# Kernel optimization log

Hardware: AMD Instinct MI355X
Metric: run time of the kernel (lower is better)

## Reference

```python
import jax, jax.numpy as jnp
import numpy as np

# Model dims (see init_kwargs)
B, S, H = 1, 1024, 2048
NH, NKV, HD = 16, 4, 128       # query heads, kv heads (GQA), head dim
RD = 64                        # partial rotary dim
E, TOPK, I = 8, 2, 1024        # experts, top-k, expert intermediate
EPS = 1e-6
THETA = 1000000.0


def setup_inputs() -> dict:
    key = jax.random.key(0)
    ks = jax.random.split(key, 12)
    s = 0.02  # init scale
    return {
        "hidden_states": jax.random.normal(ks[0], (B, S, H), jnp.float32),
        "position_ids": jnp.tile(jnp.arange(S, dtype=jnp.int32), (B, 1)),
        "ln1_w": jnp.ones((H,), jnp.float32),
        "q_norm_w": jnp.ones((NH * HD,), jnp.float32),
        "k_norm_w": jnp.ones((NKV * HD,), jnp.float32),
        "wq": jax.random.normal(ks[1], (H, NH * HD), jnp.float32) * s,
        "wk": jax.random.normal(ks[2], (H, NKV * HD), jnp.float32) * s,
        "wv": jax.random.normal(ks[3], (H, NKV * HD), jnp.float32) * s,
        "wo": jax.random.normal(ks[4], (NH * HD, H), jnp.float32) * s,
        "ln2_w": jnp.ones((H,), jnp.float32),
        "router_w": jax.random.normal(ks[5], (H, E), jnp.float32) * s,
        "router_bias": jax.random.normal(ks[6], (E,), jnp.float32) * 0.1,
        "w_gate": jax.random.normal(ks[7], (E, H, I), jnp.float32) * s,
        "w_up": jax.random.normal(ks[8], (E, H, I), jnp.float32) * s,
        "w_down": jax.random.normal(ks[9], (E, I, H), jnp.float32) * s,
    }


def rmsnorm(x, w):
    # fp32 RMSNorm over full last dim (matches DistributedRMSNorm with tp=1)
    xf = x.astype(jnp.float32)
    r = jax.lax.rsqrt(jnp.mean(xf * xf, axis=-1, keepdims=True) + EPS)
    return (xf * r * w).astype(x.dtype)


def _rope(x, cos, sin):
    # partial rotary: only first RD dims of each head are rotated
    xr, xp = x[..., :RD], x[..., RD:]
    half = RD // 2
    rot = jnp.concatenate([-xr[..., half:], xr[..., :half]], axis=-1)
    return jnp.concatenate([xr * cos + rot * sin, xp], axis=-1)


def reference(hidden_states, position_ids, ln1_w, q_norm_w, k_norm_w,
              wq, wk, wv, wo, ln2_w, router_w, router_bias,
              w_gate, w_up, w_down):
    x = hidden_states
    # --- attention block ---
    h = rmsnorm(x, ln1_w)
    Q = h @ wq  # [B,S,NH*HD]
    K = h @ wk  # [B,S,NKV*HD]
    V = h @ wv
    # MiniMax M2 qk_norm: RMSNorm over FULL projection output BEFORE head reshape
    Q = rmsnorm(Q, q_norm_w)
    K = rmsnorm(K, k_norm_w)
    q = Q.reshape(B, S, NH, HD).transpose(0, 2, 1, 3)   # [B,NH,S,HD]
    k = K.reshape(B, S, NKV, HD).transpose(0, 2, 1, 3)  # [B,NKV,S,HD]
    v = V.reshape(B, S, NKV, HD).transpose(0, 2, 1, 3)
    # partial RoPE
    inv = 1.0 / (THETA ** (jnp.arange(0, RD, 2, dtype=jnp.float32) / RD))
    ang = position_ids.astype(jnp.float32)[:, :, None] * inv  # [B,S,RD/2]
    cos = jnp.concatenate([jnp.cos(ang)] * 2, axis=-1)[:, None]  # [B,1,S,RD]
    sin = jnp.concatenate([jnp.sin(ang)] * 2, axis=-1)[:, None]
    q = _rope(q, cos, sin)
    k = _rope(k, cos, sin)
    # GQA expand
    rep = NH // NKV
    k = jnp.repeat(k, rep, axis=1)
    v = jnp.repeat(v, rep, axis=1)
    scores = jnp.einsum('bhqd,bhkd->bhqk', q, k).astype(jnp.float32) / np.sqrt(HD).astype(np.float32)
    causal = jnp.tril(jnp.ones((S, S), bool))
    scores = jnp.where(causal, scores, jnp.float32(-1e30))
    attn = jax.nn.softmax(scores, axis=-1).astype(v.dtype)
    ctx = jnp.einsum('bhqk,bhkd->bhqd', attn, v)
    attn_out = ctx.transpose(0, 2, 1, 3).reshape(B, S, NH * HD) @ wo
    res = x + attn_out
    # --- MoE block ---
    h2 = rmsnorm(res, ln2_w)
    t = h2.reshape(B * S, H)
    logits = t.astype(jnp.float32) @ router_w        # [T,E]
    sc = jax.nn.sigmoid(logits)
    # top-k chosen on bias-corrected scores; weights from uncorrected scores
    _, ti = jax.lax.top_k(sc + router_bias, TOPK)    # [T,TOPK]
    aff = jnp.take_along_axis(sc, ti, axis=-1)
    aff = aff / jnp.sum(aff, axis=-1, keepdims=True)  # normalize_top_k_affinities
    T = B * S
    combine = jnp.zeros((T, E), jnp.float32).at[jnp.arange(T)[:, None], ti].add(aff)
    # SwiGLU experts (dense-compute, sparse-combine reference for blockwise grouped GEMM)
    g = jnp.einsum('th,ehi->tei', t, w_gate)
    u = jnp.einsum('th,ehi->tei', t, w_up)
    act = jax.nn.silu(g) * u
    eo = jnp.einsum('tei,eih->teh', act, w_down)
    moe = jnp.einsum('te,teh->th', combine.astype(eo.dtype), eo)
    return res + moe.reshape(B, S, H)
```

## Files before the change

kernel.cpp:

```cpp
#include <hip/hip_runtime.h>
#include <hip/hip_bf16.h>
#include <cstdint>

static constexpr int S   = 1024;
static constexpr int H   = 2048;
static constexpr int NH  = 16;
static constexpr int NKV = 4;
static constexpr int HD  = 128;
static constexpr int EXPN = 8;
static constexpr int FFI = 1024;

typedef __bf16 bf16x8 __attribute__((ext_vector_type(8)));
typedef float  f32x4  __attribute__((ext_vector_type(4)));
typedef unsigned short ushortx8 __attribute__((ext_vector_type(8)));
typedef unsigned short ushortx4 __attribute__((ext_vector_type(4)));

#define DEVI __device__ __forceinline__

DEVI unsigned short f2bf(float f) {
    union { float f; uint32_t u; } v; v.f = f;
    uint32_t r = (v.u + 0x7FFFu + ((v.u >> 16) & 1u)) >> 16;
    return (unsigned short)r;
}
DEVI float bf2f(unsigned short s) {
    union { uint32_t u; float f; } v; v.u = ((uint32_t)s) << 16; return v.f;
}

DEVI void atomAdd(float* p, float v) { unsafeAtomicAdd(p, v); }

DEVI void gll16(const unsigned short* g, unsigned short* l) {
    __builtin_amdgcn_global_load_lds(
        (const __attribute__((address_space(1))) unsigned int*)(g),
        (__attribute__((address_space(3))) unsigned int*)(l),
        16, 0, 0);
}

template<int N> DEVI void waitvm() {
    if constexpr (N == 0)      asm volatile("s_waitcnt vmcnt(0)" ::: "memory");
    else if constexpr (N == 2) asm volatile("s_waitcnt vmcnt(2)" ::: "memory");
    else if constexpr (N == 4) asm volatile("s_waitcnt vmcnt(4)" ::: "memory");
    else if constexpr (N == 6) asm volatile("s_waitcnt vmcnt(6)" ::: "memory");
    else static_assert(N == 0 || N == 2 || N == 4 || N == 6, "unsupported vmcnt");
}
DEVI void pipe_barrier() {
    __builtin_amdgcn_sched_barrier(0);
    __builtin_amdgcn_s_barrier();
    __builtin_amdgcn_sched_barrier(0);
}

__global__ __launch_bounds__(256) void transT(const float* __restrict__ in,
                                              unsigned short* __restrict__ outp,
                                              int R, int C)
{
    __shared__ unsigned short tl[64][72];
    int zb = blockIdx.z;
    in   += (size_t)zb * R * C;
    outp += (size_t)zb * R * C;
    int c0 = blockIdx.x * 64, r0 = blockIdx.y * 64;
    int t = threadIdx.x;
    int cq = (t & 15) * 4;
    int rr = t >> 4;
    #pragma unroll
    for (int p = 0; p < 4; ++p) {
        int row = rr + p * 16;
        float4 v = *(const float4*)&in[(size_t)(r0 + row) * C + c0 + cq];
        tl[cq + 0][row] = f2bf(v.x);
        tl[cq + 1][row] = f2bf(v.y);
        tl[cq + 2][row] = f2bf(v.z);
        tl[cq + 3][row] = f2bf(v.w);
    }
    __syncthreads();
    int r8 = (t & 7) * 8;
    int cc = t >> 3;
    #pragma unroll
    for (int p = 0; p < 2; ++p) {
        int col = cc + p * 32;
        ushortx8 v = *(const ushortx8*)&tl[col][r8];
        *(ushortx8*)&outp[(size_t)(c0 + col) * R + r0 + r8] = v;
    }
}

enum { CFG_PROJ3 = 0, CFG_WO = 1, CFG_SCORES = 2, CFG_PV = 3, CFG_GATEUP = 4, CFG_DOWN = 5 };

template<int CFG, int WM, int NI, bool PIPE>
__global__ __launch_bounds__(256, 2) void gemm_k(
    const unsigned short* __restrict__ A,
    const unsigned short* __restrict__ B0,
    const unsigned short* __restrict__ B1,
    const unsigned short* __restrict__ B2,
    float* __restrict__ C0,
    float* __restrict__ C1,
    float* __restrict__ C2,
    unsigned short* __restrict__ Cb,
    const float* __restrict__ X,
    const int* __restrict__ cnt,
    const int* __restrict__ tokList,
    int arg0)
{
    constexpr bool DUAL = (CFG == CFG_GATEUP);
    constexpr int BM = WM * 32;
    constexpr int BN = NI * 32;
    constexpr int ASZ = BM * 64;
    constexpr int BSZ = BN * 64;
    constexpr int NBUF = PIPE ? 3 : 2;
    constexpr int LD = WM + NI + (DUAL ? NI : 0);

    const int tid = threadIdx.x;
    const int m0 = blockIdx.y * BM;
    int n0 = blockIdx.x * BN;

    int M = S;
    int kbeg = 0, kend = 0, LDA = 0, LDBK = 0, LDC = 0;
    const unsigned short* Ap = A;
    const unsigned short* Bb = B0;
    const unsigned short* Bb2 = B1;
    const int* tlist = nullptr;
    float* Cout = C0;
    int head = 0, e = 0, hl = 0;

    if constexpr (CFG == CFG_PROJ3) {
        int xt = blockIdx.x;
        if (xt < 32)      { Bb = B0; Cout = C0; LDC = 2048; n0 = xt * 64; }
        else if (xt < 40) { Bb = B1; Cout = C1; LDC = 512;  n0 = (xt - 32) * 64; }
        else              { Bb = B2; Cout = C2; LDC = 512;  n0 = (xt - 40) * 64; }
        LDA = H; LDBK = H; kend = H;
    } else if constexpr (CFG == CFG_WO) {
        LDA = H; LDBK = H; LDC = H; kend = H;
    } else if constexpr (CFG == CFG_SCORES) {
        hl = blockIdx.z; head = arg0 + hl;
        if (n0 >= m0 + BM) return;
        Ap = A + (size_t)head * S * HD;
        Bb = B0 + (size_t)(head >> 2) * S * HD;
        kend = HD; LDA = HD; LDBK = HD;
    } else if constexpr (CFG == CFG_PV) {
        int z = blockIdx.z; hl = z >> 2; int ks = z & 3;
        head = arg0 + hl;
        int kcap = m0 + BM;
        kbeg = ks * 256;
        if (kbeg >= kcap) return;
        kend = (kbeg + 256 < kcap) ? kbeg + 256 : kcap;
        Ap = A + (size_t)hl * S * S;
        Bb = B0 + (size_t)(head >> 2) * HD * S;
        LDA = S; LDBK = S;
    } else if constexpr (CFG == CFG_GATEUP) {
        e = blockIdx.z;
        M = cnt[e]; if (m0 >= M) return;
        tlist = tokList + e * S;
        Bb  = B0 + (size_t)e * FFI * H;
        Bb2 = B1 + (size_t)e * FFI * H;
        kend = H; LDA = H; LDBK = H;
    } else {
        e = blockIdx.z;
        M = cnt[e]; if (m0 >= M) return;
        Ap = A + (size_t)e * S * FFI;
        Bb = B0 + (size_t)e * H * FFI;
        kend = FFI; LDA = FFI; LDBK = FFI;
    }

    __shared__ unsigned short As[NBUF * ASZ];
    __shared__ unsigned short Bs[NBUF * BSZ];
    __shared__ unsigned short Bs2[DUAL ? NBUF * BSZ : 8];

    const int lane = tid & 63, grp = lane >> 4, r16 = lane & 15;
    const int wid = tid >> 6, wr = wid >> 1, wc = wid & 1;
    const int wbase8 = (tid & 0xFFC0) * 8;

    size_t aoff[WM];
    #pragma unroll
    for (int c = 0; c < WM; ++c) {
        int chunk = c * 256 + tid;
        int row = chunk >> 3;
        int kcs = (chunk & 7) * 8;
        int grow = m0 + row;
        if constexpr (CFG == CFG_GATEUP) { int r2 = grow < M ? grow : M - 1; grow = tlist[r2]; }
        else if constexpr (CFG == CFG_DOWN) { grow = grow < M ? grow : M - 1; }
        aoff[c] = (size_t)grow * LDA + (kcs ^ ((row & 7) << 3));
    }
    size_t boff[NI];
    #pragma unroll
    for (int c = 0; c < NI; ++c) {
        int chunk = c * 256 + tid;
        int row = chunk >> 3;
        int kcs = (chunk & 7) * 8;
        boff[c] = (size_t)(n0 + row) * LDBK + (kcs ^ ((row & 7) << 3));
    }

    auto STAGE = [&](int buf, int k0) {
        #pragma unroll
        for (int c = 0; c < WM; ++c)
            gll16(Ap + aoff[c] + k0, &As[buf * ASZ + c * 2048 + wbase8]);
        #pragma unroll
        for (int c = 0; c < NI; ++c)
            gll16(Bb + boff[c] + k0, &Bs[buf * BSZ + c * 2048 + wbase8]);
        if constexpr (DUAL) {
            #pragma unroll
            for (int c = 0; c < NI; ++c)
                gll16(Bb2 + boff[c] + k0, &Bs2[buf * BSZ + c * 2048 + wbase8]);
        }
    };

    f32x4 acc[WM][NI] = {};
    f32x4 acc2[DUAL ? WM : 1][DUAL ? NI : 1] = {};

    auto COMPUTE = [&](int buf) {
        #pragma unroll
        for (int kk = 0; kk < 64; kk += 32) {
            bf16x8 af[WM], bfr[NI], bfr2[DUAL ? NI : 1];
            #pragma unroll
            for (int mi = 0; mi < WM; ++mi) {
                int r = wr * (WM * 16) + mi * 16 + r16;
                int idx = buf * ASZ + r * 64 + ((kk + grp * 8) ^ ((r & 7) << 3));
                af[mi] = __builtin_bit_cast(bf16x8, *(const ushortx8*)&As[idx]);
            }
            #pragma unroll
            for (int ni = 0; ni < NI; ++ni) {
                int r = wc * (NI * 16) + ni * 16 + r16;
                int idx = buf * BSZ + r * 64 + ((kk + grp * 8) ^ ((r & 7) << 3));
                bfr[ni] = __builtin_bit_cast(bf16x8, *(const ushortx8*)&Bs[idx]);
                if constexpr (DUAL)
                    bfr2[ni] = __builtin_bit_cast(bf16x8, *(const ushortx8*)&Bs2[idx]);
            }
            #pragma unroll
            for (int mi = 0; mi < WM; ++mi)
                #pragma unroll
                for (int ni = 0; ni < NI; ++ni) {
                    acc[mi][ni] = __builtin_amdgcn_mfma_f32_16x16x32_bf16(af[mi], bfr[ni], acc[mi][ni], 0, 0, 0);
                    if constexpr (DUAL)
                        acc2[mi][ni] = __builtin_amdgcn_mfma_f32_16x16x32_bf16(af[mi], bfr2[ni], acc2[mi][ni], 0, 0, 0);
                }
        }
    };

    if constexpr (PIPE) {
        const int nk = (kend - kbeg) >> 6;
        STAGE(0, kbeg);
        if (nk > 1) STAGE(1, kbeg + 64);
        if (nk > 1) waitvm<LD>(); else waitvm<0>();
        pipe_barrier();
        int cur = 0, stg = 2;
        for (int i = 0; i < nk; ++i) {
            if (i + 2 < nk) {
                STAGE(stg, kbeg + (i + 2) * 64);
                stg = (stg == 2) ? 0 : stg + 1;
            }
            COMPUTE(cur);
            cur = (cur == 2) ? 0 : cur + 1;
            if (i + 1 < nk) {
                if (i + 2 < nk) waitvm<LD>();
                else            waitvm<0>();
                pipe_barrier();
            }
        }
    } else {
        int cur = 0;
        STAGE(0, kbeg);
        __syncthreads();
        for (int k0 = kbeg; k0 < kend; k0 += 64) {
            if (k0 + 64 < kend) STAGE(cur ^ 1, k0 + 64);
            COMPUTE(cur);
            __syncthreads();
            cur ^= 1;
        }
    }

    #pragma unroll
    for (int mi = 0; mi < WM; ++mi) {
        #pragma unroll
        for (int ni = 0; ni < NI; ++ni) {
            f32x4 v = acc[mi][ni];
            int col = n0 + wc * (NI * 16) + ni * 16 + r16;
            #pragma unroll
            for (int j = 0; j < 4; ++j) {
                int row = m0 + wr * (WM * 16) + mi * 16 + grp * 4 + j;
                float val = v[j];
                if constexpr (CFG == CFG_PROJ3) {
                    Cout[(size_t)row * LDC + col] = val;
                } else if constexpr (CFG == CFG_WO) {
                    C0[(size_t)row * H + col] = val + X[(size_t)row * H + col];
                } else if constexpr (CFG == CFG_SCORES) {
                    float sv = val * 0.08838834764831845f;
                    if (col > row) sv = -1e30f;
                    Cb[((size_t)hl * S + row) * S + col] = f2bf(sv);
                } else if constexpr (CFG == CFG_PV) {
                    atomAdd(&C0[(size_t)row * 2048 + head * HD + col], val);
                } else if constexpr (CFG == CFG_GATEUP) {
                    if (row < M) {
                        float g = val, u = acc2[mi][ni][j];
                        float a = g / (1.f + expf(-g)) * u;
                        Cb[((size_t)e * S + row) * FFI + col] = f2bf(a);
                    }
                } else {
                    if (row < M) {
                        Cb[((size_t)e * S + row) * H + col] = f2bf(val);
                    }
                }
            }
        }
    }
}

__global__ __launch_bounds__(256) void rms_h(const float* __restrict__ x,
                                             const float* __restrict__ w,
                                             unsigned short* __restrict__ out)
{
    int row = blockIdx.x, tid = threadIdx.x;
    const float* xr = x + (size_t)row * H;
    float4 a = *(const float4*)&xr[tid * 8];
    float4 b = *(const float4*)&xr[tid * 8 + 4];
    float vals[8] = { a.x, a.y, a.z, a.w, b.x, b.y, b.z, b.w };
    float ss = 0;
    #pragma unroll
    for (int j = 0; j < 8; ++j) ss += vals[j] * vals[j];
    __shared__ float red[4];
    #pragma unroll
    for (int o = 32; o; o >>= 1) ss += __shfl_down(ss, o);
    if ((tid & 63) == 0) red[tid >> 6] = ss;
    __syncthreads();
    float tot = red[0] + red[1] + red[2] + red[3];
    float r = rsqrtf(tot * (1.f / H) + 1e-6f);
    ushortx8 ov;
    #pragma unroll
    for (int j = 0; j < 8; ++j) ov[j] = f2bf(vals[j] * r * w[tid * 8 + j]);
    *(ushortx8*)&out[(size_t)row * H + tid * 8] = ov;
}

__global__ __launch_bounds__(256) void qnorm_rope(const float* __restrict__ qbuf,
                                                  const float* __restrict__ qw,
                                                  const int* __restrict__ pos,
                                                  unsigned short* __restrict__ qatt)
{
    int tok = blockIdx.x, tid = threadIdx.x;
    __shared__ float sh[2048];
    __shared__ float red[4];
    const float* xr = qbuf + (size_t)tok * 2048;
    float4 a = *(const float4*)&xr[tid * 8];
    float4 b = *(const float4*)&xr[tid * 8 + 4];
    *(float4*)&sh[tid * 8] = a;
    *(float4*)&sh[tid * 8 + 4] = b;
    float ss = a.x*a.x + a.y*a.y + a.z*a.z + a.w*a.w + b.x*b.x + b.y*b.y + b.z*b.z + b.w*b.w;
    #pragma unroll
    for (int o = 32; o; o >>= 1) ss += __shfl_down(ss, o);
    if ((tid & 63) == 0) red[tid >> 6] = ss;
    __syncthreads();
    float tot = red[0] + red[1] + red[2] + red[3];
    float r = rsqrtf(tot * (1.f / 2048.f) + 1e-6f);
    float p = (float)pos[tok];
    #pragma unroll
    for (int j = 0; j < 8; ++j) {
        int idx = tid * 8 + j;
        int d = idx & 127, hh = idx >> 7;
        float v = sh[idx] * r * qw[idx];
        float o;
        if (d < 64) {
            int jj = d & 31;
            float ang = p * expf((float)jj * -0.43173470268f);
            float c = cosf(ang), sn = sinf(ang);
            if (d < 32) { float v2 = sh[idx + 32] * r * qw[idx + 32]; o = v * c - v2 * sn; }
            else        { float v2 = sh[idx - 32] * r * qw[idx - 32]; o = v * c + v2 * sn; }
        } else o = v;
        qatt[((size_t)hh * S + tok) * HD + d] = f2bf(o);
    }
}

__global__ __launch_bounds__(256) void knorm_rope(const float* __restrict__ kbuf,
                                                  const float* __restrict__ kw,
                                                  const int* __restrict__ pos,
                                                  unsigned short* __restrict__ katt)
{
    int tok = blockIdx.x, tid = threadIdx.x;
    __shared__ float sh[512];
    __shared__ float red[4];
    const float* xr = kbuf + (size_t)tok * 512;
    float2 a = *(const float2*)&xr[tid * 2];
    sh[tid * 2] = a.x; sh[tid * 2 + 1] = a.y;
    float ss = a.x * a.x + a.y * a.y;
    #pragma unroll
    for (int o = 32; o; o >>= 1) ss += __shfl_down(ss, o);
    if ((tid & 63) == 0) red[tid >> 6] = ss;
    __syncthreads();
    float tot = red[0] + red[1] + red[2] + red[3];
    float r = rsqrtf(tot * (1.f / 512.f) + 1e-6f);
    float p = (float)pos[tok];
    #pragma unroll
    for (int j = 0; j < 2; ++j) {
        int idx = tid * 2 + j;
        int d = idx & 127, hh = idx >> 7;
        float v = sh[idx] * r * kw[idx];
        float o;
        if (d < 64) {
            int jj = d & 31;
            float ang = p * expf((float)jj * -0.43173470268f);
            float c = cosf(ang), sn = sinf(ang);
            if (d < 32) { float v2 = sh[idx + 32] * r * kw[idx + 32]; o = v * c - v2 * sn; }
            else        { float v2 = sh[idx - 32] * r * kw[idx - 32]; o = v * c + v2 * sn; }
        } else o = v;
        katt[((size_t)hh * S + tok) * HD + d] = f2bf(o);
    }
}

__global__ __launch_bounds__(256) void softmax_k(unsigned short* __restrict__ sc)
{
    int bid = blockIdx.x;
    int hl = bid >> 10, q = bid & 1023;
    unsigned short* srow = sc + ((size_t)hl * S + q) * S;
    int L = q + 1, tid = threadIdx.x;
    __shared__ float red[4];
    ushortx4 in4 = *(const ushortx4*)&srow[tid * 4];
    float v[4]; float mx = -3.4e38f;
    #pragma unroll
    for (int i = 0; i < 4; ++i) {
        int j = tid * 4 + i;
        if (j < L) { v[i] = bf2f(in4[i]); mx = fmaxf(mx, v[i]); }
        else v[i] = -3.4e38f;
    }
    float m = mx;
    #pragma unroll
    for (int o = 32; o; o >>= 1) m = fmaxf(m, __shfl_down(m, o));
    if ((tid & 63) == 0) red[tid >> 6] = m;
    __syncthreads();
    float M_ = fmaxf(fmaxf(red[0], red[1]), fmaxf(red[2], red[3]));
    __syncthreads();
    float e[4]; float sum = 0;
    #pragma unroll
    for (int i = 0; i < 4; ++i) {
        int j = tid * 4 + i;
        if (j < L) { e[i] = expf(v[i] - M_); sum += e[i]; } else e[i] = 0.f;
    }
    #pragma unroll
    for (int o = 32; o; o >>= 1) sum += __shfl_down(sum, o);
    if ((tid & 63) == 0) red[tid >> 6] = sum;
    __syncthreads();
    float inv = 1.f / (red[0] + red[1] + red[2] + red[3]);
    ushortx4 o4;
    #pragma unroll
    for (int i = 0; i < 4; ++i) o4[i] = f2bf(e[i] * inv);
    *(ushortx4*)&srow[tid * 4] = o4;
}

__global__ void zero_cnt(int* cnt) { if (threadIdx.x < EXPN) cnt[threadIdx.x] = 0; }

__global__ void zerok(float4* __restrict__ p, int n4)
{
    int i = blockIdx.x * 256 + threadIdx.x;
    if (i < n4) p[i] = float4{0.f, 0.f, 0.f, 0.f};
}

__global__ void cvt_k(const float* __restrict__ src, unsigned short* __restrict__ dst)
{
    int i = blockIdx.x * 256 + threadIdx.x;
    float4 a = *(const float4*)&src[i * 8];
    float4 b = *(const float4*)&src[i * 8 + 4];
    float v[8] = { a.x, a.y, a.z, a.w, b.x, b.y, b.z, b.w };
    ushortx8 o;
    #pragma unroll
    for (int j = 0; j < 8; ++j) o[j] = f2bf(v[j]);
    *(ushortx8*)&dst[i * 8] = o;
}

__global__ __launch_bounds__(256) void router_k(const float* __restrict__ res,
                                                const float* __restrict__ ln2w,
                                                const float* __restrict__ rw,
                                                const float* __restrict__ rbias,
                                                int* __restrict__ cnt,
                                                int* __restrict__ tokList,
                                                int* __restrict__ slot,
                                                float* __restrict__ slotw,
                                                unsigned short* __restrict__ tbf)
{
    int tok = blockIdx.x, tid = threadIdx.x;
    const float* xr = res + (size_t)tok * H;
    float4 a = *(const float4*)&xr[tid * 8];
    float4 b = *(const float4*)&xr[tid * 8 + 4];
    float vals[8] = { a.x, a.y, a.z, a.w, b.x, b.y, b.z, b.w };
    float ss = 0;
    #pragma unroll
    for (int j = 0; j < 8; ++j) ss += vals[j] * vals[j];
    __shared__ float red[4];
    float t_ = ss;
    #pragma unroll
    for (int o = 32; o; o >>= 1) t_ += __shfl_down(t_, o);
    if ((tid & 63) == 0) red[tid >> 6] = t_;
    __syncthreads();
    float tot = red[0] + red[1] + red[2] + red[3];
    float r = rsqrtf(tot * (1.f / H) + 1e-6f);

    float acc[EXPN] = {};
    ushortx8 tv8;
    #pragma unroll
    for (int j = 0; j < 8; ++j) {
        float tv = vals[j] * r * ln2w[tid * 8 + j];
        tv8[j] = f2bf(tv);
        const float* rp = rw + (size_t)(tid * 8 + j) * EXPN;
        #pragma unroll
        for (int e = 0; e < EXPN; ++e) acc[e] += tv * rp[e];
    }
    *(ushortx8*)&tbf[(size_t)tok * H + tid * 8] = tv8;
    __shared__ float r8[4][EXPN];
    #pragma unroll
    for (int e = 0; e < EXPN; ++e) {
        float s_ = acc[e];
        #pragma unroll
        for (int o = 32; o; o >>= 1) s_ += __shfl_down(s_, o);
        acc[e] = s_;
    }
    if ((tid & 63) == 0)
        for (int e = 0; e < EXPN; ++e) r8[tid >> 6][e] = acc[e];
    __syncthreads();
    if (tid == 0) {
        float sg[EXPN];
        for (int e = 0; e < EXPN; ++e) {
            float lg = r8[0][e] + r8[1][e] + r8[2][e] + r8[3][e];
            sg[e] = 1.f / (1.f + expf(-lg));
        }
        int i0 = 0; float b0 = -1e30f;
        for (int e = 0; e < EXPN; ++e) {
            float s_ = sg[e] + rbias[e];
            if (s_ > b0) { b0 = s_; i0 = e; }
        }
        int i1 = -1; float b1 = -1e30f;
        for (int e = 0; e < EXPN; ++e) {
            if (e == i0) continue;
            float s_ = sg[e] + rbias[e];
            if (s_ > b1) { b1 = s_; i1 = e; }
        }
        float a0 = sg[i0], a1 = sg[i1], inv = 1.f / (a0 + a1);
        int p0 = atomicAdd(&cnt[i0], 1);
        tokList[i0 * S + p0] = tok;
        int p1 = atomicAdd(&cnt[i1], 1);
        tokList[i1 * S + p1] = tok;
        slot[tok * 2]     = i0 * S + p0;  slotw[tok * 2]     = a0 * inv;
        slot[tok * 2 + 1] = i1 * S + p1;  slotw[tok * 2 + 1] = a1 * inv;
    }
}

__global__ __launch_bounds__(256) void combine_k(const unsigned short* __restrict__ eo,
                                                 const int* __restrict__ slot,
                                                 const float* __restrict__ slotw,
                                                 float* __restrict__ out)
{
    int t = blockIdx.x;
    int c = threadIdx.x * 8;
    int s0 = slot[t * 2], s1 = slot[t * 2 + 1];
    float w0 = slotw[t * 2], w1 = slotw[t * 2 + 1];
    ushortx8 a = *(const ushortx8*)&eo[(size_t)s0 * H + c];
    ushortx8 b = *(const ushortx8*)&eo[(size_t)s1 * H + c];
    size_t base = (size_t)t * H + c;
    float4 o0 = *(float4*)&out[base];
    float4 o1 = *(float4*)&out[base + 4];
    float ov[8] = { o0.x, o0.y, o0.z, o0.w, o1.x, o1.y, o1.z, o1.w };
    #pragma unroll
    for (int j = 0; j < 8; ++j)
        ov[j] += w0 * bf2f(a[j]) + w1 * bf2f(b[j]);
    *(float4*)&out[base]     = float4{ ov[0], ov[1], ov[2], ov[3] };
    *(float4*)&out[base + 4] = float4{ ov[4], ov[5], ov[6], ov[7] };
}

extern "C" void kernel_launch(void* const* d_in, const int* in_sizes, int n_in,
                              void* d_out, int out_size, void* d_ws, size_t ws_size,
                              hipStream_t stream)
{
    const float* x     = (const float*)d_in[0];
    const int*   pos   = (const int*)d_in[1];
    const float* ln1w  = (const float*)d_in[2];
    const float* qnw   = (const float*)d_in[3];
    const float* knw   = (const float*)d_in[4];
    const float* wq    = (const float*)d_in[5];
    const float* wk    = (const float*)d_in[6];
    const float* wv    = (const float*)d_in[7];
    const float* wo    = (const float*)d_in[8];
    const float* ln2w  = (const float*)d_in[9];
    const float* rw    = (const float*)d_in[10];
    const float* rbias = (const float*)d_in[11];
    const float* wg    = (const float*)d_in[12];
    const float* wu    = (const float*)d_in[13];
    const float* wd    = (const float*)d_in[14];
    float* out = (float*)d_out;

    char* ws = (char*)d_ws;
    const size_t MB = 1024 * 1024;
    unsigned short* h_bf = (unsigned short*)(ws + 0);
    float* qbuf  = (float*)(ws + 4 * MB);
    float* ctxf  = (float*)(ws + 4 * MB);
    float* kbuf  = (float*)(ws + 12 * MB);
    float* vbuf  = (float*)(ws + 14 * MB);
    unsigned short* qatt = (unsigned short*)(ws + 16 * MB);
    unsigned short* katt = (unsigned short*)(ws + 20 * MB);
    unsigned short* vT   = (unsigned short*)(ws + 21 * MB);
    unsigned short* ctx  = (unsigned short*)(ws + 22 * MB);
    unsigned short* tbf  = (unsigned short*)(ws + 26 * MB);
    int*   cnt     = (int*)(ws + 30 * MB);
    int*   tokList = (int*)(ws + 30 * MB + 4096);
    int*   slot    = (int*)(ws + 30 * MB + 512 * 1024);
    float* slotw   = (float*)(ws + 30 * MB + 768 * 1024);
    unsigned short* scores = (unsigned short*)(ws + 31 * MB);
    unsigned short* act = (unsigned short*)(ws + 31 * MB);
    unsigned short* eo  = (unsigned short*)(ws + 47 * MB);
    unsigned short* wqT = (unsigned short*)(ws + 79 * MB);
    unsigned short* wkT = (unsigned short*)(ws + 87 * MB);
    unsigned short* wvT = (unsigned short*)(ws + 89 * MB);
    unsigned short* woT = (unsigned short*)(ws + 91 * MB);
    unsigned short* wgT = (unsigned short*)(ws + 99 * MB);
    unsigned short* wuT = (unsigned short*)(ws + 131 * MB);
    unsigned short* wdT = (unsigned short*)(ws + 163 * MB);

    transT<<<dim3(32, 32, 1), 256, 0, stream>>>(wq, wqT, 2048, 2048);
    transT<<<dim3(8,  32, 1), 256, 0, stream>>>(wk, wkT, 2048, 512);
    transT<<<dim3(8,  32, 1), 256, 0, stream>>>(wv, wvT, 2048, 512);
    transT<<<dim3(32, 32, 1), 256, 0, stream>>>(wo, woT, 2048, 2048);
    transT<<<dim3(16, 32, 8), 256, 0, stream>>>(wg, wgT, 2048, 1024);
    transT<<<dim3(16, 32, 8), 256, 0, stream>>>(wu, wuT, 2048, 1024);
    transT<<<dim3(32, 16, 8), 256, 0, stream>>>(wd, wdT, 1024, 2048);

    rms_h<<<S, 256, 0, stream>>>(x, ln1w, h_bf);

    gemm_k<CFG_PROJ3, 2, 2, true><<<dim3(48, 16, 1), 256, 0, stream>>>(h_bf, wqT, wkT, wvT, qbuf, kbuf, vbuf, nullptr, nullptr, nullptr, nullptr, 0);

    qnorm_rope<<<S, 256, 0, stream>>>(qbuf, qnw, pos, qatt);
    knorm_rope<<<S, 256, 0, stream>>>(kbuf, knw, pos, katt);
    transT<<<dim3(8, 16, 1), 256, 0, stream>>>(vbuf, vT, 1024, 512);
    zerok<<<2048, 256, 0, stream>>>((float4*)ctxf, (8 * MB) / 16);

    gemm_k<CFG_SCORES, 2, 4, false><<<dim3(8, 16, 16), 256, 0, stream>>>(qatt, katt, nullptr, nullptr, nullptr, nullptr, nullptr, scores, nullptr, nullptr, nullptr, 0);
    softmax_k<<<16 * S, 256, 0, stream>>>(scores);
    gemm_k<CFG_PV, 2, 2, true><<<dim3(2, 16, 64), 256, 0, stream>>>(scores, vT, nullptr, nullptr, ctxf, nullptr, nullptr, nullptr, nullptr, nullptr, nullptr, 0);
    cvt_k<<<(S * 2048) / (256 * 8), 256, 0, stream>>>(ctxf, ctx);

    gemm_k<CFG_WO, 2, 2, true><<<dim3(32, 16, 1), 256, 0, stream>>>(ctx, woT, nullptr, nullptr, out, nullptr, nullptr, nullptr, x, nullptr, nullptr, 0);

    zero_cnt<<<1, 64, 0, stream>>>(cnt);
    router_k<<<S, 256, 0, stream>>>(out, ln2w, rw, rbias, cnt, tokList, slot, slotw, tbf);

    gemm_k<CFG_GATEUP, 2, 2, false><<<dim3(16, 16, EXPN), 256, 0, stream>>>(tbf, wgT, wuT, nullptr, nullptr, nullptr, nullptr, act, nullptr, cnt, tokList, 0);
    gemm_k<CFG_DOWN, 2, 2, true><<<dim3(32, 16, EXPN), 256, 0, stream>>>(act, wdT, nullptr, nullptr, nullptr, nullptr, nullptr, eo, nullptr, cnt, tokList, 0);
    combine_k<<<S, 256, 0, stream>>>(eo, slot, slotw, out);
}
```

Before: 332.1 us.

## Load gathered A rows directly into registers for gate/up GEMM and enable pipelining

For the MoE gate/up GEMM, the gathered token rows of A are now read straight from global memory into MFMA fragment registers per wave, skipping the LDS staging buffer. The kernel also switches this GEMM to the 3-buffer pipelined path, with the wait counts adjusted to cover only the B loads. This removes LDS traffic and shared-memory footprint for A and can raise occupancy. The cost is that each wave redundantly loads A rows shared with other waves in the same row, and the direct loads are synchronous global reads issued just before compute, so their latency may be exposed.

```diff
diff --git a/kernel.cpp b/kernel.cpp
--- a/kernel.cpp
+++ b/kernel.cpp
@@ -98,12 +98,13 @@
     int arg0)
 {
     constexpr bool DUAL = (CFG == CFG_GATEUP);
+    constexpr bool AREG = (CFG == CFG_GATEUP);
     constexpr int BM = WM * 32;
     constexpr int BN = NI * 32;
     constexpr int ASZ = BM * 64;
     constexpr int BSZ = BN * 64;
     constexpr int NBUF = PIPE ? 3 : 2;
-    constexpr int LD = WM + NI + (DUAL ? NI : 0);
+    constexpr int LD = AREG ? (2 * NI) : (WM + NI + (DUAL ? NI : 0));
 
     const int tid = threadIdx.x;
     const int m0 = blockIdx.y * BM;
@@ -157,7 +158,7 @@
         kend = FFI; LDA = FFI; LDBK = FFI;
     }
 
-    __shared__ unsigned short As[NBUF * ASZ];
+    __shared__ unsigned short As[AREG ? 8 : NBUF * ASZ];
     __shared__ unsigned short Bs[NBUF * BSZ];
     __shared__ unsigned short Bs2[DUAL ? NBUF * BSZ : 8];
 
@@ -166,15 +167,24 @@
     const int wbase8 = (tid & 0xFFC0) * 8;
 
     size_t aoff[WM];
-    #pragma unroll
-    for (int c = 0; c < WM; ++c) {
-        int chunk = c * 256 + tid;
-        int row = chunk >> 3;
-        int kcs = (chunk & 7) * 8;
-        int grow = m0 + row;
-        if constexpr (CFG == CFG_GATEUP) { int r2 = grow < M ? grow : M - 1; grow = tlist[r2]; }
-        else if constexpr (CFG == CFG_DOWN) { grow = grow < M ? grow : M - 1; }
-        aoff[c] = (size_t)grow * LDA + (kcs ^ ((row & 7) << 3));
+    const unsigned short* aptr[AREG ? WM : 1];
+    if constexpr (AREG) {
+        #pragma unroll
+        for (int mi = 0; mi < WM; ++mi) {
+            int row = wr * (WM * 16) + mi * 16 + r16;
+            int gr = m0 + row; if (gr >= M) gr = M - 1;
+            aptr[mi] = Ap + (size_t)tlist[gr] * LDA + grp * 8;
+        }
+    } else {
+        #pragma unroll
+        for (int c = 0; c < WM; ++c) {
+            int chunk = c * 256 + tid;
+            int row = chunk >> 3;
+            int kcs = (chunk & 7) * 8;
+            int grow = m0 + row;
+            if constexpr (CFG == CFG_DOWN) { grow = grow < M ? grow : M - 1; }
+            aoff[c] = (size_t)grow * LDA + (kcs ^ ((row & 7) << 3));
+        }
     }
     size_t boff[NI];
     #pragma unroll
@@ -186,9 +196,11 @@
     }
 
     auto STAGE = [&](int buf, int k0) {
-        #pragma unroll
-        for (int c = 0; c < WM; ++c)
-            gll16(Ap + aoff[c] + k0, &As[buf * ASZ + c * 2048 + wbase8]);
+        if constexpr (!AREG) {
+            #pragma unroll
+            for (int c = 0; c < WM; ++c)
+                gll16(Ap + aoff[c] + k0, &As[buf * ASZ + c * 2048 + wbase8]);
+        }
         #pragma unroll
         for (int c = 0; c < NI; ++c)
             gll16(Bb + boff[c] + k0, &Bs[buf * BSZ + c * 2048 + wbase8]);
@@ -201,6 +213,17 @@
 
     f32x4 acc[WM][NI] = {};
     f32x4 acc2[DUAL ? WM : 1][DUAL ? NI : 1] = {};
+    bf16x8 afg[AREG ? WM : 1][AREG ? 2 : 1];
+
+    auto LOAD_A = [&](int k0) {
+        if constexpr (AREG) {
+            #pragma unroll
+            for (int mi = 0; mi < WM; ++mi)
+                #pragma unroll
+                for (int t2 = 0; t2 < 2; ++t2)
+                    afg[mi][t2] = __builtin_bit_cast(bf16x8, *(const ushortx8*)(aptr[mi] + k0 + t2 * 32));
+        }
+    };
 
     auto COMPUTE = [&](int buf) {
         #pragma unroll
@@ -208,9 +231,13 @@
             bf16x8 af[WM], bfr[NI], bfr2[DUAL ? NI : 1];
             #pragma unroll
             for (int mi = 0; mi < WM; ++mi) {
-                int r = wr * (WM * 16) + mi * 16 + r16;
-                int idx = buf * ASZ + r * 64 + ((kk + grp * 8) ^ ((r & 7) << 3));
-                af[mi] = __builtin_bit_cast(bf16x8, *(const ushortx8*)&As[idx]);
+                if constexpr (AREG) {
+                    af[mi] = afg[mi][kk >> 5];
+                } else {
+                    int r = wr * (WM * 16) + mi * 16 + r16;
+                    int idx = buf * ASZ + r * 64 + ((kk + grp * 8) ^ ((r & 7) << 3));
+                    af[mi] = __builtin_bit_cast(bf16x8, *(const ushortx8*)&As[idx]);
+                }
             }
             #pragma unroll
             for (int ni = 0; ni < NI; ++ni) {
@@ -239,6 +266,8 @@
         pipe_barrier();
         int cur = 0, stg = 2;
         for (int i = 0; i < nk; ++i) {
+            LOAD_A(kbeg + i * 64);
+            if constexpr (AREG) __builtin_amdgcn_sched_barrier(0);
             if (i + 2 < nk) {
                 STAGE(stg, kbeg + (i + 2) * 64);
                 stg = (stg == 2) ? 0 : stg + 1;
@@ -256,6 +285,7 @@
         STAGE(0, kbeg);
         __syncthreads();
         for (int k0 = kbeg; k0 < kend; k0 += 64) {
+            LOAD_A(k0);
             if (k0 + 64 < kend) STAGE(cur ^ 1, k0 + 64);
             COMPUTE(cur);
             __syncthreads();
@@ -630,7 +660,7 @@
     zero_cnt<<<1, 64, 0, stream>>>(cnt);
     router_k<<<S, 256, 0, stream>>>(out, ln2w, rw, rbias, cnt, tokList, slot, slotw, tbf);
 
-    gemm_k<CFG_GATEUP, 2, 2, false><<<dim3(16, 16, EXPN), 256, 0, stream>>>(tbf, wgT, wuT, nullptr, nullptr, nullptr, nullptr, act, nullptr, cnt, tokList, 0);
+    gemm_k<CFG_GATEUP, 2, 2, true><<<dim3(16, 16, EXPN), 256, 0, stream>>>(tbf, wgT, wuT, nullptr, nullptr, nullptr, nullptr, act, nullptr, cnt, tokList, 0);
     gemm_k<CFG_DOWN, 2, 2, true><<<dim3(32, 16, EXPN), 256, 0, stream>>>(act, wdT, nullptr, nullptr, nullptr, nullptr, nullptr, eo, nullptr, cnt, tokList, 0);
     combine_k<<<S, 256, 0, stream>>>(eo, slot, slotw, out);
 }
```

Result: slower. 355.7 us (+7.1%).
